# Performance work log

Hardware: AMD Instinct MI355X
Metric: run time of the kernel (lower is better)

## Reference

```python
import jax, jax.numpy as jnp
import numpy as np

N_NODES = 50000
IN_CH = 128
OUT_CH = 64
N_EDGES = 800000


def setup_inputs() -> dict:
    key = jax.random.key(0)
    k_x, k_e, k_w, k_b = jax.random.split(key, 4)
    x = jax.random.normal(k_x, (N_NODES, IN_CH), dtype=jnp.float32)
    edge_index = jax.random.randint(k_e, (2, N_EDGES), 0, N_NODES, dtype=jnp.int64)
    # nn.Linear(in, out, bias=False): weight [out, in], applied as x @ W^T
    W = jax.random.normal(k_w, (OUT_CH, IN_CH), dtype=jnp.float32) * (1.0 / np.sqrt(IN_CH))
    bias = jax.random.normal(k_b, (OUT_CH,), dtype=jnp.float32) * 0.02
    return {"x": x, "edge_index": edge_index, "W": W, "bias": bias}


def reference(x, edge_index, W, bias):
    # linear projection (no bias): [N, in] @ [in, out] -> [N, out]
    h = x @ W.T
    src = edge_index[0]
    dst = edge_index[1]
    # gather source node feats per edge: [E, out]
    msgs = h[src]
    # scatter_add into dest nodes: [N, out]
    out = jax.ops.segment_sum(msgs, dst, num_segments=h.shape[0])
    return out + bias
```

## Files before the change

kernel.cpp:

```cpp
#include <hip/hip_runtime.h>

#define IN_CH 128
#define OUT_CH 64
#define TN 64
#define XS_STRIDE 132
#define WS_STRIDE 129

#define PBLOCKS 512
#define NB 800
#define CAPA 8
#define DCAP 32

__device__ __forceinline__ unsigned f2bf(float f) {
    unsigned u = __float_as_uint(f);
    return (u + 0x7FFFu + ((u >> 16) & 1u)) >> 16;
}

__device__ __forceinline__ void fma4(float4& acc, float s, const float4& wv) {
    acc.x += s * wv.x;
    acc.y += s * wv.y;
    acc.z += s * wv.z;
    acc.w += s * wv.w;
}

__global__ __launch_bounds__(256) void k_gemm(const float* __restrict__ x,
                                              const float* __restrict__ W,
                                              unsigned* __restrict__ h16,
                                              int* __restrict__ spillCount,
                                              int nNodes) {
    __shared__ float smem[TN * XS_STRIDE + IN_CH * OUT_CH];
    float* u  = smem;
    float* wt = smem + TN * XS_STRIDE;

    int tid = threadIdx.x;
    int nodeBase = blockIdx.x * TN;
    if (blockIdx.x == 0 && tid == 0) *spillCount = 0;

    {
        const float4* W4 = (const float4*)W;
        for (int i = tid; i < IN_CH * OUT_CH / 4; i += 256) {
            float4 v = W4[i];
            int o = i >> 5;
            int k = (i & 31) * 4;
            float* d = u + o * WS_STRIDE + k;
            d[0] = v.x; d[1] = v.y; d[2] = v.z; d[3] = v.w;
        }
    }
    __syncthreads();
    {
        int o = tid & 63;
        int k0 = (tid >> 6) * 32;
#pragma unroll 8
        for (int k = k0; k < k0 + 32; ++k)
            wt[k * OUT_CH + o] = u[o * WS_STRIDE + k];
    }
    __syncthreads();
    {
        int remRows = nNodes - nodeBase;
        if (remRows > TN) remRows = TN;
        const float4* X4 = (const float4*)(x + (size_t)nodeBase * IN_CH);
        for (int i = tid; i < TN * IN_CH / 4; i += 256) {
            int r = i >> 5;
            int k = (i & 31) * 4;
            float4 v = make_float4(0.f, 0.f, 0.f, 0.f);
            if (r < remRows) v = X4[i];
            *(float4*)(u + r * XS_STRIDE + k) = v;
        }
    }
    __syncthreads();

    int tx = tid & 15;
    int ty = tid >> 4;

    float4 acc[4];
#pragma unroll
    for (int i = 0; i < 4; ++i) acc[i] = make_float4(0.f, 0.f, 0.f, 0.f);

    const float* wcol = wt + tx * 4;
#pragma unroll 4
    for (int k = 0; k < IN_CH; k += 4) {
        float4 w0 = *(const float4*)(wcol + (k + 0) * OUT_CH);
        float4 w1 = *(const float4*)(wcol + (k + 1) * OUT_CH);
        float4 w2 = *(const float4*)(wcol + (k + 2) * OUT_CH);
        float4 w3 = *(const float4*)(wcol + (k + 3) * OUT_CH);
#pragma unroll
        for (int i = 0; i < 4; ++i) {
            float4 a = *(const float4*)(u + (ty * 4 + i) * XS_STRIDE + k);
            fma4(acc[i], a.x, w0);
            fma4(acc[i], a.y, w1);
            fma4(acc[i], a.z, w2);
            fma4(acc[i], a.w, w3);
        }
    }

#pragma unroll
    for (int i = 0; i < 4; ++i) {
        int n = nodeBase + ty * 4 + i;
        if (n < nNodes) {
            uint2 pk;
            pk.x = f2bf(acc[i].x) | (f2bf(acc[i].y) << 16);
            pk.y = f2bf(acc[i].z) | (f2bf(acc[i].w) << 16);
            *(uint2*)(h16 + (size_t)n * 32 + tx * 2) = pk;
        }
    }
}

__global__ __launch_bounds__(256) void k_partA(const int* __restrict__ ei,
                                               unsigned* __restrict__ cells,
                                               int* __restrict__ cntA,
                                               uint2* __restrict__ spill,
                                               int* __restrict__ spillCount,
                                               int nEdges, int nNodes) {
    __shared__ unsigned lists[NB * CAPA];
    __shared__ int curs[NB];
    __shared__ int is64s;
    int tid = threadIdx.x;
    for (int i = tid; i < NB; i += 256) curs[i] = 0;
    if (tid == 0) {
        int v = 1;
#pragma unroll
        for (int j = 0; j < 16; ++j)
            if (ei[2 * j + 1] != 0) v = 0;
        is64s = v;
    }
    __syncthreads();
    int is64 = is64s;

    int chunk = (nEdges + PBLOCKS - 1) / PBLOCKS;
    int e0 = blockIdx.x * chunk;
    int e1 = min(e0 + chunk, nEdges);
    for (int e = e0 + tid; e < e1; e += 256) {
        int src, dst;
        if (is64) {
            src = ((const int2*)ei)[e].x;
            dst = ((const int2*)ei)[nEdges + e].x;
        } else {
            src = ei[e];
            dst = ei[nEdges + e];
        }
        if ((unsigned)src >= (unsigned)nNodes) src = 0;
        if ((unsigned)dst >= (unsigned)nNodes) dst = 0;
        int bucket = dst >> 6;
        int rank = (bucket < NB) ? atomicAdd(&curs[bucket], 1) : CAPA;
        if (rank < CAPA) {
            lists[bucket * CAPA + rank] = (unsigned)src | ((unsigned)(dst & 63) << 16);
        } else {
            int sp = atomicAdd(spillCount, 1);
            if (sp < nEdges) spill[sp] = make_uint2((unsigned)src, (unsigned)dst);
        }
    }
    __syncthreads();

    size_t base = (size_t)blockIdx.x * NB;
    uint4* cells4 = (uint4*)(cells + base * CAPA);
    for (int j = tid; j < NB * CAPA / 4; j += 256)
        cells4[j] = *(const uint4*)(lists + 4 * j);
    for (int i = tid; i < NB; i += 256)
        cntA[base + i] = min(curs[i], CAPA);
}

__global__ __launch_bounds__(256) void k_partB(const unsigned* __restrict__ cells,
                                               const int* __restrict__ cntA,
                                               int* __restrict__ slots,
                                               int* __restrict__ cntB,
                                               uint2* __restrict__ spill,
                                               int* __restrict__ spillCount,
                                               int nNodes, int nEdges) {
    __shared__ unsigned nl[64 * DCAP];
    __shared__ int nc[64];
    int tid = threadIdx.x;
    int b = blockIdx.x;
    int nodeBase = b * 64;

    if (b >= NB) {
        for (int i = tid; i < 64; i += 256)
            cntB[nodeBase + i] = 0;
        return;
    }

    if (tid < 64) nc[tid] = 0;
    __syncthreads();

    for (int blk = tid; blk < PBLOCKS; blk += 256) {
        int c = cntA[(size_t)blk * NB + b];
        const unsigned* cb = cells + ((size_t)blk * NB + b) * CAPA;
        uint4 w0 = *(const uint4*)(cb + 0);
        uint4 w1 = *(const uint4*)(cb + 4);
        unsigned w[CAPA] = {w0.x, w0.y, w0.z, w0.w, w1.x, w1.y, w1.z, w1.w};
#pragma unroll
        for (int r = 0; r < CAPA; ++r) {
            if (r < c) {
                unsigned rec = w[r];
                int sub = (int)(rec >> 16);
                int rank = atomicAdd(&nc[sub], 1);
                if (rank < DCAP) {
                    nl[sub * DCAP + rank] = rec & 0xFFFFu;
                } else {
                    int sp = atomicAdd(spillCount, 1);
                    if (sp < nEdges) spill[sp] = make_uint2(rec & 0xFFFFu, (unsigned)(nodeBase + sub));
                }
            }
        }
    }
    __syncthreads();

    uint4* s4 = (uint4*)(slots + (size_t)nodeBase * DCAP);
    for (int j = tid; j < 64 * DCAP / 4; j += 256)
        s4[j] = *(const uint4*)(nl + 4 * j);
    for (int i = tid; i < 64; i += 256)
        cntB[nodeBase + i] = min(nc[i], DCAP);
}

__global__ __launch_bounds__(256) void k_gather(const int* __restrict__ cnt,
                                                const int* __restrict__ slots,
                                                const unsigned* __restrict__ h16,
                                                const float* __restrict__ bias,
                                                float* __restrict__ out, int nNodes) {
    int tid = blockIdx.x * 256 + threadIdx.x;
    int node = tid >> 6;
    if (node >= nNodes) return;
    int lane = tid & 63;
    int half = lane >> 5;
    int cp   = lane & 31;

    int d = cnt[node];
    if (d < 0) d = 0;
    if (d > DCAP) d = DCAP;
    int jend = (d + 1) & ~1;

    int myslot = (lane < d) ? slots[node * DCAP + lane] : 0;

    float2 acc = {0.f, 0.f};
    int j = half;
    for (; j + 6 < jend; j += 8) {
        int s0 = __shfl(myslot, j, 64);
        int s1 = __shfl(myslot, j + 2, 64);
        int s2 = __shfl(myslot, j + 4, 64);
        int s3 = __shfl(myslot, j + 6, 64);
        unsigned v0 = h16[(size_t)s0 * 32 + cp];
        unsigned v1 = h16[(size_t)s1 * 32 + cp];
        unsigned v2 = h16[(size_t)s2 * 32 + cp];
        unsigned v3 = h16[(size_t)s3 * 32 + cp];
        if (j + 6 >= d) v3 = 0;
        acc.x += __uint_as_float(v0 << 16);
        acc.y += __uint_as_float(v0 & 0xFFFF0000u);
        acc.x += __uint_as_float(v1 << 16);
        acc.y += __uint_as_float(v1 & 0xFFFF0000u);
        acc.x += __uint_as_float(v2 << 16);
        acc.y += __uint_as_float(v2 & 0xFFFF0000u);
        acc.x += __uint_as_float(v3 << 16);
        acc.y += __uint_as_float(v3 & 0xFFFF0000u);
    }
    for (; j < jend; j += 2) {
        int s = __shfl(myslot, j, 64);
        unsigned v = h16[(size_t)s * 32 + cp];
        if (j >= d) v = 0;
        acc.x += __uint_as_float(v << 16);
        acc.y += __uint_as_float(v & 0xFFFF0000u);
    }

    acc.x += __shfl_down(acc.x, 32, 64);
    acc.y += __shfl_down(acc.y, 32, 64);
    if (half == 0) {
        float2 bv = *(const float2*)(bias + cp * 2);
        float2 o;
        o.x = acc.x + bv.x;
        o.y = acc.y + bv.y;
        *(float2*)(out + (size_t)node * OUT_CH + cp * 2) = o;
    }
}

__global__ __launch_bounds__(256) void k_spill(const uint2* __restrict__ spill,
                                               const int* __restrict__ spillCount,
                                               const unsigned* __restrict__ h16,
                                               float* __restrict__ out, int nEdges) {
    int n = *spillCount;
    if (n > nEdges) n = nEdges;
    long long total = (long long)n * 32;
    for (long long t = blockIdx.x * 256 + threadIdx.x; t < total; t += (long long)gridDim.x * 256) {
        int e = (int)(t >> 5);
        int cp = (int)(t & 31);
        uint2 sd = spill[e];
        unsigned v = h16[(size_t)sd.x * 32 + cp];
        float* o = out + (size_t)sd.y * OUT_CH + cp * 2;
        unsafeAtomicAdd(o + 0, __uint_as_float(v << 16));
        unsafeAtomicAdd(o + 1, __uint_as_float(v & 0xFFFF0000u));
    }
}

extern "C" void kernel_launch(void* const* d_in, const int* in_sizes, int n_in,
                              void* d_out, int out_size, void* d_ws, size_t ws_size,
                              hipStream_t stream) {
    const float* x    = (const float*)d_in[0];
    const int*   ei   = (const int*)d_in[1];
    const float* W    = (const float*)d_in[2];
    const float* bias = (const float*)d_in[3];
    float* out = (float*)d_out;

    int nNodes = in_sizes[0] / IN_CH;
    int nEdges = in_sizes[1] / 2;
    int realBuckets = (nNodes + 63) / 64;
    int padNodes = realBuckets * 64;

    char* p = (char*)d_ws;
    auto alloc = [&](size_t bytes) {
        char* r = p;
        p += (bytes + 255) & ~(size_t)255;
        return r;
    };
    unsigned* h16        = (unsigned*)alloc((size_t)nNodes * 32 * sizeof(unsigned));
    unsigned* cells      = (unsigned*)alloc((size_t)PBLOCKS * NB * CAPA * sizeof(unsigned));
    int*      cntA       = (int*)alloc((size_t)PBLOCKS * NB * sizeof(int));
    int*      slots      = (int*)alloc((size_t)padNodes * DCAP * sizeof(int));
    int*      cntB       = (int*)alloc((size_t)padNodes * sizeof(int));
    uint2*    spill      = (uint2*)alloc((size_t)nEdges * sizeof(uint2));
    int*      spillCount = (int*)alloc(sizeof(int));

    k_gemm<<<(nNodes + TN - 1) / TN, 256, 0, stream>>>(x, W, h16, spillCount, nNodes);
    k_partA<<<PBLOCKS, 256, 0, stream>>>(ei, cells, cntA, spill, spillCount, nEdges, nNodes);
    k_partB<<<realBuckets, 256, 0, stream>>>(cells, cntA, slots, cntB, spill, spillCount, nNodes, nEdges);
    k_gather<<<(nNodes * OUT_CH + 255) / 256, 256, 0, stream>>>(cntB, slots, h16, bias, out, nNodes);
    k_spill<<<64, 256, 0, stream>>>(spill, spillCount, h16, out, nEdges);
}
```

Baseline: 144.0 us.

## Fuse GEMM with partition A and partition B with gather into two kernels

The projection GEMM and the first edge-partition pass now run as one launch, with the blocks split by index, so the two independent stages can overlap on the device. The second partition pass and the per-node gather are merged into a 1024-thread kernel that keeps each node's neighbour list in shared memory instead of writing slots and counts to global memory and reading them back. The spill counter is reset with a memset because the first kernel's blocks no longer have a defined order. This saves two launches and a global round trip, at the cost of larger blocks and fewer of them in the gather phase, which can lower occupancy.

```diff
diff --git a/kernel.cpp b/kernel.cpp
--- a/kernel.cpp
+++ b/kernel.cpp
@@ -23,18 +23,71 @@
     acc.w += s * wv.w;
 }
 
-__global__ __launch_bounds__(256) void k_gemm(const float* __restrict__ x,
-                                              const float* __restrict__ W,
-                                              unsigned* __restrict__ h16,
-                                              int* __restrict__ spillCount,
-                                              int nNodes) {
+__global__ __launch_bounds__(256) void k_fusedA(const float* __restrict__ x,
+                                                const float* __restrict__ W,
+                                                unsigned* __restrict__ h16,
+                                                const int* __restrict__ ei,
+                                                unsigned* __restrict__ cells,
+                                                int* __restrict__ cntA,
+                                                uint2* __restrict__ spill,
+                                                int* __restrict__ spillCount,
+                                                int nNodes, int nEdges, int gemmBlocks) {
     __shared__ float smem[TN * XS_STRIDE + IN_CH * OUT_CH];
+    __shared__ int is64s;
+    int tid = threadIdx.x;
+
+    if (blockIdx.x >= gemmBlocks) {
+        unsigned* lists = (unsigned*)smem;
+        int* curs = (int*)smem + NB * CAPA;
+        int pblk = blockIdx.x - gemmBlocks;
+        for (int i = tid; i < NB; i += 256) curs[i] = 0;
+        if (tid == 0) {
+            int v = 1;
+#pragma unroll
+            for (int j = 0; j < 16; ++j)
+                if (ei[2 * j + 1] != 0) v = 0;
+            is64s = v;
+        }
+        __syncthreads();
+        int is64 = is64s;
+
+        int chunk = (nEdges + PBLOCKS - 1) / PBLOCKS;
+        int e0 = pblk * chunk;
+        int e1 = min(e0 + chunk, nEdges);
+        for (int e = e0 + tid; e < e1; e += 256) {
+            int src, dst;
+            if (is64) {
+                src = ((const int2*)ei)[e].x;
+                dst = ((const int2*)ei)[nEdges + e].x;
+            } else {
+                src = ei[e];
+                dst = ei[nEdges + e];
+            }
+            if ((unsigned)src >= (unsigned)nNodes) src = 0;
+            if ((unsigned)dst >= (unsigned)nNodes) dst = 0;
+            int bucket = dst >> 6;
+            int rank = (bucket < NB) ? atomicAdd(&curs[bucket], 1) : CAPA;
+            if (rank < CAPA) {
+                lists[bucket * CAPA + rank] = (unsigned)src | ((unsigned)(dst & 63) << 16);
+            } else {
+                int sp = atomicAdd(spillCount, 1);
+                if (sp < nEdges) spill[sp] = make_uint2((unsigned)src, (unsigned)dst);
+            }
+        }
+        __syncthreads();
+
+        size_t base = (size_t)pblk * NB;
+        uint4* cells4 = (uint4*)(cells + base * CAPA);
+        for (int j = tid; j < NB * CAPA / 4; j += 256)
+            cells4[j] = *(const uint4*)(lists + 4 * j);
+        for (int i = tid; i < NB; i += 256)
+            cntA[base + i] = min(curs[i], CAPA);
+        return;
+    }
+
     float* u  = smem;
     float* wt = smem + TN * XS_STRIDE;
-
-    int tid = threadIdx.x;
     int nodeBase = blockIdx.x * TN;
-    if (blockIdx.x == 0 && tid == 0) *spillCount = 0;
 
     {
         const float4* W4 = (const float4*)W;
@@ -105,168 +158,103 @@
     }
 }
 
-__global__ __launch_bounds__(256) void k_partA(const int* __restrict__ ei,
-                                               unsigned* __restrict__ cells,
-                                               int* __restrict__ cntA,
-                                               uint2* __restrict__ spill,
-                                               int* __restrict__ spillCount,
-                                               int nEdges, int nNodes) {
-    __shared__ unsigned lists[NB * CAPA];
-    __shared__ int curs[NB];
-    __shared__ int is64s;
-    int tid = threadIdx.x;
-    for (int i = tid; i < NB; i += 256) curs[i] = 0;
-    if (tid == 0) {
-        int v = 1;
-#pragma unroll
-        for (int j = 0; j < 16; ++j)
-            if (ei[2 * j + 1] != 0) v = 0;
-        is64s = v;
-    }
-    __syncthreads();
-    int is64 = is64s;
-
-    int chunk = (nEdges + PBLOCKS - 1) / PBLOCKS;
-    int e0 = blockIdx.x * chunk;
-    int e1 = min(e0 + chunk, nEdges);
-    for (int e = e0 + tid; e < e1; e += 256) {
-        int src, dst;
-        if (is64) {
-            src = ((const int2*)ei)[e].x;
-            dst = ((const int2*)ei)[nEdges + e].x;
-        } else {
-            src = ei[e];
-            dst = ei[nEdges + e];
-        }
-        if ((unsigned)src >= (unsigned)nNodes) src = 0;
-        if ((unsigned)dst >= (unsigned)nNodes) dst = 0;
-        int bucket = dst >> 6;
-        int rank = (bucket < NB) ? atomicAdd(&curs[bucket], 1) : CAPA;
-        if (rank < CAPA) {
-            lists[bucket * CAPA + rank] = (unsigned)src | ((unsigned)(dst & 63) << 16);
-        } else {
-            int sp = atomicAdd(spillCount, 1);
-            if (sp < nEdges) spill[sp] = make_uint2((unsigned)src, (unsigned)dst);
-        }
-    }
-    __syncthreads();
-
-    size_t base = (size_t)blockIdx.x * NB;
-    uint4* cells4 = (uint4*)(cells + base * CAPA);
-    for (int j = tid; j < NB * CAPA / 4; j += 256)
-        cells4[j] = *(const uint4*)(lists + 4 * j);
-    for (int i = tid; i < NB; i += 256)
-        cntA[base + i] = min(curs[i], CAPA);
-}
-
-__global__ __launch_bounds__(256) void k_partB(const unsigned* __restrict__ cells,
-                                               const int* __restrict__ cntA,
-                                               int* __restrict__ slots,
-                                               int* __restrict__ cntB,
-                                               uint2* __restrict__ spill,
-                                               int* __restrict__ spillCount,
-                                               int nNodes, int nEdges) {
+__global__ __launch_bounds__(1024) void k_fusedB(const unsigned* __restrict__ cells,
+                                                 const int* __restrict__ cntA,
+                                                 const unsigned* __restrict__ h16,
+                                                 const float* __restrict__ bias,
+                                                 float* __restrict__ out,
+                                                 uint2* __restrict__ spill,
+                                                 int* __restrict__ spillCount,
+                                                 int nNodes, int nEdges) {
     __shared__ unsigned nl[64 * DCAP];
     __shared__ int nc[64];
     int tid = threadIdx.x;
     int b = blockIdx.x;
     int nodeBase = b * 64;
 
-    if (b >= NB) {
-        for (int i = tid; i < 64; i += 256)
-            cntB[nodeBase + i] = 0;
-        return;
-    }
-
     if (tid < 64) nc[tid] = 0;
     __syncthreads();
 
-    for (int blk = tid; blk < PBLOCKS; blk += 256) {
-        int c = cntA[(size_t)blk * NB + b];
-        const unsigned* cb = cells + ((size_t)blk * NB + b) * CAPA;
-        uint4 w0 = *(const uint4*)(cb + 0);
-        uint4 w1 = *(const uint4*)(cb + 4);
-        unsigned w[CAPA] = {w0.x, w0.y, w0.z, w0.w, w1.x, w1.y, w1.z, w1.w};
-#pragma unroll
-        for (int r = 0; r < CAPA; ++r) {
-            if (r < c) {
-                unsigned rec = w[r];
-                int sub = (int)(rec >> 16);
-                int rank = atomicAdd(&nc[sub], 1);
-                if (rank < DCAP) {
-                    nl[sub * DCAP + rank] = rec & 0xFFFFu;
-                } else {
-                    int sp = atomicAdd(spillCount, 1);
-                    if (sp < nEdges) spill[sp] = make_uint2(rec & 0xFFFFu, (unsigned)(nodeBase + sub));
+    if (b < NB) {
+        for (int blk = tid; blk < PBLOCKS; blk += 1024) {
+            int c = cntA[(size_t)blk * NB + b];
+            const unsigned* cb = cells + ((size_t)blk * NB + b) * CAPA;
+            uint4 w0 = *(const uint4*)(cb + 0);
+            uint4 w1 = *(const uint4*)(cb + 4);
+            unsigned w[CAPA] = {w0.x, w0.y, w0.z, w0.w, w1.x, w1.y, w1.z, w1.w};
+#pragma unroll
+            for (int r = 0; r < CAPA; ++r) {
+                if (r < c) {
+                    unsigned rec = w[r];
+                    int sub = (int)(rec >> 16);
+                    int rank = atomicAdd(&nc[sub], 1);
+                    if (rank < DCAP) {
+                        nl[sub * DCAP + rank] = rec & 0xFFFFu;
+                    } else {
+                        int sp = atomicAdd(spillCount, 1);
+                        if (sp < nEdges) spill[sp] = make_uint2(rec & 0xFFFFu, (unsigned)(nodeBase + sub));
+                    }
                 }
             }
         }
     }
     __syncthreads();
 
-    uint4* s4 = (uint4*)(slots + (size_t)nodeBase * DCAP);
-    for (int j = tid; j < 64 * DCAP / 4; j += 256)
-        s4[j] = *(const uint4*)(nl + 4 * j);
-    for (int i = tid; i < 64; i += 256)
-        cntB[nodeBase + i] = min(nc[i], DCAP);
-}
-
-__global__ __launch_bounds__(256) void k_gather(const int* __restrict__ cnt,
-                                                const int* __restrict__ slots,
-                                                const unsigned* __restrict__ h16,
-                                                const float* __restrict__ bias,
-                                                float* __restrict__ out, int nNodes) {
-    int tid = blockIdx.x * 256 + threadIdx.x;
-    int node = tid >> 6;
-    if (node >= nNodes) return;
     int lane = tid & 63;
+    int wv   = tid >> 6;
     int half = lane >> 5;
     int cp   = lane & 31;
-
-    int d = cnt[node];
-    if (d < 0) d = 0;
-    if (d > DCAP) d = DCAP;
-    int jend = (d + 1) & ~1;
-
-    int myslot = (lane < d) ? slots[node * DCAP + lane] : 0;
-
-    float2 acc = {0.f, 0.f};
-    int j = half;
-    for (; j + 6 < jend; j += 8) {
-        int s0 = __shfl(myslot, j, 64);
-        int s1 = __shfl(myslot, j + 2, 64);
-        int s2 = __shfl(myslot, j + 4, 64);
-        int s3 = __shfl(myslot, j + 6, 64);
-        unsigned v0 = h16[(size_t)s0 * 32 + cp];
-        unsigned v1 = h16[(size_t)s1 * 32 + cp];
-        unsigned v2 = h16[(size_t)s2 * 32 + cp];
-        unsigned v3 = h16[(size_t)s3 * 32 + cp];
-        if (j + 6 >= d) v3 = 0;
-        acc.x += __uint_as_float(v0 << 16);
-        acc.y += __uint_as_float(v0 & 0xFFFF0000u);
-        acc.x += __uint_as_float(v1 << 16);
-        acc.y += __uint_as_float(v1 & 0xFFFF0000u);
-        acc.x += __uint_as_float(v2 << 16);
-        acc.y += __uint_as_float(v2 & 0xFFFF0000u);
-        acc.x += __uint_as_float(v3 << 16);
-        acc.y += __uint_as_float(v3 & 0xFFFF0000u);
-    }
-    for (; j < jend; j += 2) {
-        int s = __shfl(myslot, j, 64);
-        unsigned v = h16[(size_t)s * 32 + cp];
-        if (j >= d) v = 0;
-        acc.x += __uint_as_float(v << 16);
-        acc.y += __uint_as_float(v & 0xFFFF0000u);
-    }
-
-    acc.x += __shfl_down(acc.x, 32, 64);
-    acc.y += __shfl_down(acc.y, 32, 64);
-    if (half == 0) {
-        float2 bv = *(const float2*)(bias + cp * 2);
-        float2 o;
-        o.x = acc.x + bv.x;
-        o.y = acc.y + bv.y;
-        *(float2*)(out + (size_t)node * OUT_CH + cp * 2) = o;
+    float2 bv = *(const float2*)(bias + cp * 2);
+
+#pragma unroll
+    for (int i = 0; i < 4; ++i) {
+        int sub = wv * 4 + i;
+        int node = nodeBase + sub;
+        if (node >= nNodes) continue;
+
+        int d = nc[sub];
+        if (d > DCAP) d = DCAP;
+        int jend = (d + 1) & ~1;
+
+        int myslot = (lane < d) ? (int)nl[sub * DCAP + lane] : 0;
+
+        float2 acc = {0.f, 0.f};
+        int j = half;
+        for (; j + 6 < jend; j += 8) {
+            int s0 = __shfl(myslot, j, 64);
+            int s1 = __shfl(myslot, j + 2, 64);
+            int s2 = __shfl(myslot, j + 4, 64);
+            int s3 = __shfl(myslot, j + 6, 64);
+            unsigned v0 = h16[(size_t)s0 * 32 + cp];
+            unsigned v1 = h16[(size_t)s1 * 32 + cp];
+            unsigned v2 = h16[(size_t)s2 * 32 + cp];
+            unsigned v3 = h16[(size_t)s3 * 32 + cp];
+            if (j + 6 >= d) v3 = 0;
+            acc.x += __uint_as_float(v0 << 16);
+            acc.y += __uint_as_float(v0 & 0xFFFF0000u);
+            acc.x += __uint_as_float(v1 << 16);
+            acc.y += __uint_as_float(v1 & 0xFFFF0000u);
+            acc.x += __uint_as_float(v2 << 16);
+            acc.y += __uint_as_float(v2 & 0xFFFF0000u);
+            acc.x += __uint_as_float(v3 << 16);
+            acc.y += __uint_as_float(v3 & 0xFFFF0000u);
+        }
+        for (; j < jend; j += 2) {
+            int s = __shfl(myslot, j, 64);
+            unsigned v = h16[(size_t)s * 32 + cp];
+            if (j >= d) v = 0;
+            acc.x += __uint_as_float(v << 16);
+            acc.y += __uint_as_float(v & 0xFFFF0000u);
+        }
+
+        acc.x += __shfl_down(acc.x, 32, 64);
+        acc.y += __shfl_down(acc.y, 32, 64);
+        if (half == 0) {
+            float2 o;
+            o.x = acc.x + bv.x;
+            o.y = acc.y + bv.y;
+            *(float2*)(out + (size_t)node * OUT_CH + cp * 2) = o;
+        }
     }
 }
 
@@ -299,8 +287,8 @@
 
     int nNodes = in_sizes[0] / IN_CH;
     int nEdges = in_sizes[1] / 2;
+    int gemmBlocks = (nNodes + TN - 1) / TN;
     int realBuckets = (nNodes + 63) / 64;
-    int padNodes = realBuckets * 64;
 
     char* p = (char*)d_ws;
     auto alloc = [&](size_t bytes) {
@@ -311,14 +299,13 @@
     unsigned* h16        = (unsigned*)alloc((size_t)nNodes * 32 * sizeof(unsigned));
     unsigned* cells      = (unsigned*)alloc((size_t)PBLOCKS * NB * CAPA * sizeof(unsigned));
     int*      cntA       = (int*)alloc((size_t)PBLOCKS * NB * sizeof(int));
-    int*      slots      = (int*)alloc((size_t)padNodes * DCAP * sizeof(int));
-    int*      cntB       = (int*)alloc((size_t)padNodes * sizeof(int));
     uint2*    spill      = (uint2*)alloc((size_t)nEdges * sizeof(uint2));
     int*      spillCount = (int*)alloc(sizeof(int));
 
-    k_gemm<<<(nNodes + TN - 1) / TN, 256, 0, stream>>>(x, W, h16, spillCount, nNodes);
-    k_partA<<<PBLOCKS, 256, 0, stream>>>(ei, cells, cntA, spill, spillCount, nEdges, nNodes);
-    k_partB<<<realBuckets, 256, 0, stream>>>(cells, cntA, slots, cntB, spill, spillCount, nNodes, nEdges);
-    k_gather<<<(nNodes * OUT_CH + 255) / 256, 256, 0, stream>>>(cntB, slots, h16, bias, out, nNodes);
+    hipMemsetAsync(spillCount, 0, sizeof(int), stream);
+    k_fusedA<<<gemmBlocks + PBLOCKS, 256, 0, stream>>>(x, W, h16, ei, cells, cntA,
+                                                       spill, spillCount, nNodes, nEdges, gemmBlocks);
+    k_fusedB<<<realBuckets, 1024, 0, stream>>>(cells, cntA, h16, bias, out,
+                                               spill, spillCount, nNodes, nEdges);
     k_spill<<<64, 256, 0, stream>>>(spill, spillCount, h16, out, nEdges);
 }
```

New measurement: 138.3 us. -4.0%, faster.
